# Optimization experiments

Measured on AMD Instinct MI355X. Metric: run time of the kernel, lower is better.

## Reference

```python
import jax, jax.numpy as jnp
import numpy as np

B_, L, D_MODEL = 2, 2048, 1024
EXPAND, D_INNER, D_STATE, DT_RANK, D_CONV = 2, 2048, 16, 64, 4
DT_MIN, DT_MAX = 0.001, 0.1


def setup_inputs() -> dict:
    key = jax.random.key(0)
    ks = jax.random.split(key, 8)
    s = lambda fan: 1.0 / np.sqrt(fan)
    # S4D-real style init for A: A = -exp(A_log), A_log = log(1..n) repeated over d_inner
    A0 = jnp.broadcast_to(jnp.arange(1, D_STATE + 1, dtype=jnp.float32), (D_INNER, D_STATE))
    return {
        "x": jax.random.normal(ks[0], (B_, L, D_MODEL), jnp.float32),
        "W_in": jax.random.normal(ks[1], (D_MODEL, 2 * D_INNER), jnp.float32) * s(D_MODEL),
        "conv_k": jax.random.normal(ks[2], (D_CONV, D_INNER // EXPAND, D_INNER), jnp.float32) * s(D_CONV * D_INNER // EXPAND),
        "conv_b": jnp.zeros((D_INNER,), jnp.float32),
        "W_x": jax.random.normal(ks[3], (D_INNER, DT_RANK + 2 * D_STATE), jnp.float32) * s(D_INNER),
        "W_dt": jax.random.normal(ks[4], (DT_RANK, D_INNER), jnp.float32) * s(DT_RANK),
        "b_dt": jnp.zeros((D_INNER,), jnp.float32),
        "A_log": jnp.log(A0),
        "D": jnp.ones((D_INNER,), jnp.float32),
        "W_out": jax.random.normal(ks[5], (D_INNER, D_MODEL), jnp.float32) * s(D_INNER),
    }


def reference(x, W_in, conv_k, conv_b, W_x, W_dt, b_dt, A_log, D, W_out):
    # in_proj -> split into ssm branch and gating residual branch
    xz = x @ W_in                                   # (b, l, 2*d_inner)
    xs, res = jnp.split(xz, 2, axis=-1)
    # causal grouped conv1d (feature_group_count = expand)
    xc = jax.lax.conv_general_dilated(
        xs, conv_k, window_strides=(1,), padding=[(D_CONV - 1, 0)],
        dimension_numbers=("NWC", "WIO", "NWC"), feature_group_count=EXPAND,
    ) + conv_b
    u = jax.nn.silu(xc)                             # (b, l, d_inner)
    # x_proj -> delta(low-rank), B, C
    dbc = u @ W_x                                   # (b, l, dt_rank + 2n)
    dt_raw = dbc[..., :DT_RANK]
    Bm = dbc[..., DT_RANK:DT_RANK + D_STATE]        # (b, l, n)
    Cm = dbc[..., DT_RANK + D_STATE:]               # (b, l, n)
    delta = jax.nn.softplus(dt_raw @ W_dt + b_dt)   # (b, l, d_inner)
    delta = jnp.clip(delta, DT_MIN, DT_MAX)
    A = -jnp.exp(A_log)                             # (d_inner, n)
    dA = jnp.exp(delta[..., None] * A)              # (b, l, d_inner, n)
    dBu = delta[..., None] * u[..., None] * Bm[:, :, None, :]  # (b, l, d_inner, n)

    def step(h, inp):
        dA_t, dBu_t, C_t = inp                      # (b,d,n),(b,d,n),(b,n)
        h = dA_t * h + dBu_t
        y_t = jnp.einsum('bdn,bn->bd', h, C_t)
        return h, y_t

    h0 = jnp.zeros((x.shape[0], D_INNER, D_STATE), dA.dtype)
    _, y = jax.lax.scan(step, h0, (dA.transpose(1, 0, 2, 3), dBu.transpose(1, 0, 2, 3), Cm.transpose(1, 0, 2)))
    y = y.transpose(1, 0, 2) + u * D                # (b, l, d_inner)
    out = (y * jax.nn.silu(res)) @ W_out            # (b, l, d_model)
    return out
```

## Files before the change

kernel.cpp:

```cpp
#include <hip/hip_runtime.h>
#include <math.h>


typedef unsigned short ushort_t;
typedef unsigned int uint_t;
typedef __bf16 bf16x8 __attribute__((ext_vector_type(8)));
typedef float floatx4 __attribute__((ext_vector_type(4)));

#define LDS_STRIDE 40

#define GLOAD16(gp, lp) \
    __builtin_amdgcn_global_load_lds((const __attribute__((address_space(1))) void*)(gp), \
                                     (__attribute__((address_space(3))) void*)(lp), 16, 0, 0)

__device__ __forceinline__ float silu_f(float x) { return x / (1.0f + __expf(-x)); }

__device__ __forceinline__ unsigned short f2bf(float f) {
    unsigned u = __float_as_uint(f);
    unsigned r = u + 0x7fffu + ((u >> 16) & 1u);
    return (unsigned short)(r >> 16);
}
__device__ __forceinline__ float bf2f(unsigned short h) {
    return __uint_as_float(((unsigned)h) << 16);
}
__device__ __forceinline__ uint_t packhl(float v) {
    const unsigned short h = f2bf(v);
    const unsigned short l = f2bf(v - bf2f(h));
    return (uint_t)h | ((uint_t)l << 16);
}
__device__ __forceinline__ float unpack_sum(uint_t pk) {
    return __uint_as_float(pk << 16) + __uint_as_float(pk & 0xffff0000u);
}
__device__ __forceinline__ void unpack8(uint4 w0, uint4 w1, uint4& H, uint4& L) {
    H.x = (w0.x & 0xffffu) | (w0.y << 16);  L.x = (w0.x >> 16) | (w0.y & 0xffff0000u);
    H.y = (w0.z & 0xffffu) | (w0.w << 16);  L.y = (w0.z >> 16) | (w0.w & 0xffff0000u);
    H.z = (w1.x & 0xffffu) | (w1.y << 16);  L.z = (w1.x >> 16) | (w1.y & 0xffff0000u);
    H.w = (w1.z & 0xffffu) | (w1.w << 16);  L.w = (w1.z >> 16) | (w1.w & 0xffff0000u);
}
__device__ __forceinline__ size_t faddr(int n, int k, int KC) {
    return ((size_t)((n >> 4) * KC + (k >> 5)) * 64 + (n & 15) + (((k >> 3) & 3) << 4)) * 8
           + (k & 7);
}

__global__ __launch_bounds__(256) void prep_all(
    const float* __restrict__ x, const float* __restrict__ W_in,
    const float* __restrict__ conv_k, const float* __restrict__ W_out,
    const float* __restrict__ W_x,
    ushort_t* __restrict__ xh, ushort_t* __restrict__ xl,
    ushort_t* __restrict__ WinF, ushort_t* __restrict__ convkF,
    ushort_t* __restrict__ WoutF, ushort_t* __restrict__ WxF,
    ushort_t* __restrict__ XSP_h)
{
    __shared__ float ts[32][33];
    const int bid = blockIdx.x;
    const int t = threadIdx.x;
    if (bid < 4096) {
        const size_t i4 = ((size_t)bid * 256 + t) * 4;
        float4 v = *(const float4*)&x[i4];
        ushort4 h, l;
        h.x = f2bf(v.x); l.x = f2bf(v.x - bf2f(h.x));
        h.y = f2bf(v.y); l.y = f2bf(v.y - bf2f(h.y));
        h.z = f2bf(v.z); l.z = f2bf(v.z - bf2f(h.z));
        h.w = f2bf(v.w); l.w = f2bf(v.w - bf2f(h.w));
        *(ushort4*)&xh[i4] = h;
        *(ushort4*)&xl[i4] = l;
        return;
    }
    if (bid >= 18432 && bid < 19456) {
        const int idx = (bid - 18432) * 256 + t;
        const int r = idx >> 11, k = idx & 2047;
        float v = (r < 96) ? W_x[(size_t)k * 96 + r] : 0.f;
        WxF[faddr(r, k, 64)] = f2bf(v);
        return;
    }
    if (bid >= 19456) {
        const int idx = (bid - 19456) * 256 + t;
        const int b = idx / 6144, rem = idx % 6144;
        const int lp = rem >> 11, c = rem & 2047;
        XSP_h[((size_t)b * 2051 + lp) * 2048 + c] = 0;
        return;
    }
    const float* src; int R, C, KC; ushort_t* dst; int bx, by;
    if (bid < 8192)       { src = W_in;   R = 1024; C = 4096; KC = 32;  dst = WinF;
                            int l = bid - 4096;  bx = l & 127; by = l >> 7; }
    else if (bid < 16384) { src = conv_k; R = 4096; C = 2048; KC = 128; dst = convkF;
                            int l = bid - 8192;  bx = l & 63;  by = l >> 6; }
    else                  { src = W_out;  R = 2048; C = 1024; KC = 64;  dst = WoutF;
                            int l = bid - 16384; bx = l & 31;  by = l >> 5; }
    const int tx = t & 31, ty = t >> 5;
    const int r0 = by * 32, c0 = bx * 32;
    #pragma unroll
    for (int j = 0; j < 4; ++j)
        ts[ty + j * 8][tx] = src[(size_t)(r0 + ty + j * 8) * C + c0 + tx];
    __syncthreads();
    #pragma unroll
    for (int j = 0; j < 4; ++j) {
        const int n = c0 + ty + j * 8, k = r0 + tx;
        dst[faddr(n, k, KC)] = f2bf(ts[tx][ty + j * 8]);
    }
}

template<int MODE>
__global__ __launch_bounds__(256) void gemm2(
    const uint_t* __restrict__ Apk, const ushort_t* __restrict__ Bf, int Kfull,
    float* __restrict__ Cf, ushort_t* __restrict__ Oh)
{
    __shared__ __align__(16) ushort_t As_h[128 * LDS_STRIDE];
    __shared__ __align__(16) ushort_t As_l[128 * LDS_STRIDE];
    const int t = threadIdx.x;
    int bx, by;
    if (MODE == 2) { bx = blockIdx.x; by = blockIdx.y; }
    else {
        const int lin = blockIdx.x, xcd = lin & 7, s = lin >> 3;
        bx = s >> 2;
        by = xcd * 4 + (s & 3);
    }
    const int m0 = by * 128;
    const int n0 = (MODE == 2) ? 0 : bx * 128;
    const int kbeg = (MODE == 2) ? bx * 512 : 0;
    const int kend = (MODE == 2) ? kbeg + 512 : Kfull;
    const int KC = Kfull >> 5;
    const int lane = t & 63, wave = t >> 6;
    const int wm = (wave >> 1) * 64, wn = (wave & 1) * 64;
    const int m16 = lane & 15, q = lane >> 4;
    const int n16b = (n0 + wn) >> 4;
    const int r_0 = t >> 2, cc_0 = (t & 3) * 8;
    const int r_1 = (t + 256) >> 2, cc_1 = ((t + 256) & 3) * 8;

    uint4 a00 = *(const uint4*)&Apk[(size_t)(m0 + r_0) * Kfull + kbeg + cc_0];
    uint4 a01 = *(const uint4*)&Apk[(size_t)(m0 + r_0) * Kfull + kbeg + cc_0 + 4];
    uint4 a10 = *(const uint4*)&Apk[(size_t)(m0 + r_1) * Kfull + kbeg + cc_1];
    uint4 a11 = *(const uint4*)&Apk[(size_t)(m0 + r_1) * Kfull + kbeg + cc_1 + 4];
    bf16x8 bc[4];
    {
        const int kc = kbeg >> 5;
        #pragma unroll
        for (int j = 0; j < 4; ++j)
            bc[j] = *(const bf16x8*)&Bf[(((size_t)(n16b + j) * KC + kc) * 64 + lane) * 8];
    }

    floatx4 acc[4][4];
    const floatx4 zz = {0.f, 0.f, 0.f, 0.f};
    #pragma unroll
    for (int i = 0; i < 4; ++i)
        #pragma unroll
        for (int j = 0; j < 4; ++j) acc[i][j] = zz;

    for (int k0 = kbeg; k0 < kend; k0 += 32) {
        uint4 H, L;
        unpack8(a00, a01, H, L);
        *(uint4*)&As_h[r_0 * LDS_STRIDE + cc_0] = H;
        *(uint4*)&As_l[r_0 * LDS_STRIDE + cc_0] = L;
        unpack8(a10, a11, H, L);
        *(uint4*)&As_h[r_1 * LDS_STRIDE + cc_1] = H;
        *(uint4*)&As_l[r_1 * LDS_STRIDE + cc_1] = L;
        __syncthreads();
        bf16x8 bn[4];
        if (k0 + 32 < kend) {
            const int kn = k0 + 32, kc = kn >> 5;
            a00 = *(const uint4*)&Apk[(size_t)(m0 + r_0) * Kfull + kn + cc_0];
            a01 = *(const uint4*)&Apk[(size_t)(m0 + r_0) * Kfull + kn + cc_0 + 4];
            a10 = *(const uint4*)&Apk[(size_t)(m0 + r_1) * Kfull + kn + cc_1];
            a11 = *(const uint4*)&Apk[(size_t)(m0 + r_1) * Kfull + kn + cc_1 + 4];
            #pragma unroll
            for (int j = 0; j < 4; ++j)
                bn[j] = *(const bf16x8*)&Bf[(((size_t)(n16b + j) * KC + kc) * 64 + lane) * 8];
        }
        bf16x8 ah[4], al[4];
        #pragma unroll
        for (int i = 0; i < 4; ++i) {
            const int off = (wm + i * 16 + m16) * LDS_STRIDE + q * 8;
            ah[i] = *(const bf16x8*)&As_h[off];
            al[i] = *(const bf16x8*)&As_l[off];
        }
        #pragma unroll
        for (int i = 0; i < 4; ++i)
            #pragma unroll
            for (int j = 0; j < 4; ++j) {
                acc[i][j] = __builtin_amdgcn_mfma_f32_16x16x32_bf16(ah[i], bc[j], acc[i][j], 0, 0, 0);
                acc[i][j] = __builtin_amdgcn_mfma_f32_16x16x32_bf16(al[i], bc[j], acc[i][j], 0, 0, 0);
            }
        #pragma unroll
        for (int j = 0; j < 4; ++j) bc[j] = bn[j];
        __syncthreads();
    }

    float* Cp = (MODE == 2) ? (Cf + (size_t)bx * 393216) : Cf;
    #pragma unroll
    for (int i = 0; i < 4; ++i) {
        const int row_b = m0 + wm + i * 16 + q * 4;
        #pragma unroll
        for (int j = 0; j < 4; ++j) {
            const int col = n0 + wn + j * 16 + m16;
            #pragma unroll
            for (int rr = 0; rr < 4; ++rr) {
                const int row = row_b + rr;
                const float v = acc[i][j][rr];
                if (MODE == 1) {
                    Cp[(size_t)row * 1024 + col] = v;
                } else {
                    if (col < 96) Cp[(size_t)row * 96 + col] = v;
                }
            }
        }
    }
}

__global__ __launch_bounds__(512, 4) void gemm0p(
    const ushort_t* __restrict__ Ahp, const ushort_t* __restrict__ Alp,
    const ushort_t* __restrict__ Bf,
    float* __restrict__ RES, ushort_t* __restrict__ XSP)
{
    __shared__ __align__(16) ushort_t AhS[2][128 * 32];
    __shared__ __align__(16) ushort_t AlS[2][128 * 32];
    __shared__ __align__(16) ushort_t BS[2][8 * 512];
    const int t = threadIdx.x;
    const int lin = blockIdx.x, xcd = lin & 7, s = lin >> 3;
    const int by = (xcd >> 1) * 8 + (s & 7);
    const int bx = (xcd & 1) * 16 + (s >> 3);
    const int m0 = by * 128, n0 = bx * 128;
    const int lane = t & 63, wave = t >> 6;
    const int wm = (wave >> 2) * 64, wn = (wave & 3) * 32;
    const int m16 = lane & 15, q = lane >> 4;
    const int n16base = n0 >> 4;
    const int l16 = lane >> 2;
    const int csA = (lane & 3) ^ ((lane >> 3) & 3);

    auto stageT = [&](int dbuf, int kc) {
        const int r0 = wave * 16;
        const size_t ga = (size_t)(m0 + r0 + l16) * 1024 + kc * 32 + csA * 8;
        GLOAD16(Ahp + ga, &AhS[dbuf][r0 * 32]);
        GLOAD16(Alp + ga, &AlS[dbuf][r0 * 32]);
        const size_t gb = ((size_t)(n16base + wave) * 32 + kc) * 512 + lane * 8;
        GLOAD16(Bf + gb, &BS[dbuf][wave * 512]);
    };

    floatx4 acc[4][2];
    const floatx4 zz = {0.f, 0.f, 0.f, 0.f};
    #pragma unroll
    for (int i = 0; i < 4; ++i)
        #pragma unroll
        for (int j = 0; j < 2; ++j) acc[i][j] = zz;

    stageT(0, 0);
    asm volatile("s_waitcnt vmcnt(0)" ::: "memory");
    __builtin_amdgcn_s_barrier();
    asm volatile("" ::: "memory");

    int cur = 0;
    for (int T = 0; T < 32; ++T) {
        const int nxt = cur ^ 1;
        if (T < 31) {
            stageT(nxt, T + 1);
            asm volatile("s_waitcnt vmcnt(3)" ::: "memory");
        } else {
            asm volatile("s_waitcnt vmcnt(0)" ::: "memory");
        }
        __builtin_amdgcn_s_barrier();
        asm volatile("" ::: "memory");
        bf16x8 ah[4], al[4], bb[2];
        #pragma unroll
        for (int mi = 0; mi < 4; ++mi) {
            const int rr2 = wm + mi * 16 + m16;
            const int ch = q ^ ((m16 >> 1) & 3);
            ah[mi] = *(const bf16x8*)&AhS[cur][rr2 * 32 + ch * 8];
            al[mi] = *(const bf16x8*)&AlS[cur][rr2 * 32 + ch * 8];
        }
        #pragma unroll
        for (int j = 0; j < 2; ++j)
            bb[j] = *(const bf16x8*)&BS[cur][((wn >> 4) + j) * 512 + lane * 8];
        __builtin_amdgcn_s_setprio(1);
        #pragma unroll
        for (int mi = 0; mi < 4; ++mi)
            #pragma unroll
            for (int j = 0; j < 2; ++j) {
                acc[mi][j] = __builtin_amdgcn_mfma_f32_16x16x32_bf16(ah[mi], bb[j], acc[mi][j], 0, 0, 0);
                acc[mi][j] = __builtin_amdgcn_mfma_f32_16x16x32_bf16(al[mi], bb[j], acc[mi][j], 0, 0, 0);
            }
        __builtin_amdgcn_s_setprio(0);
        asm volatile("" ::: "memory");
        __builtin_amdgcn_s_barrier();
        asm volatile("" ::: "memory");
        cur = nxt;
    }

    #pragma unroll
    for (int i = 0; i < 4; ++i) {
        const int row_b = m0 + wm + i * 16 + q * 4;
        #pragma unroll
        for (int j = 0; j < 2; ++j) {
            const int col = n0 + wn + j * 16 + m16;
            #pragma unroll
            for (int rr = 0; rr < 4; ++rr) {
                const int row = row_b + rr;
                const float v = acc[i][j][rr];
                if (n0 < 2048) {
                    const int b = row >> 11, l = row & 2047;
                    XSP[((size_t)b * 2051 + l + 3) * 2048 + col] = f2bf(v);
                } else {
                    RES[(size_t)row * 2048 + (col - 2048)] = v;
                }
            }
        }
    }
}

__global__ __launch_bounds__(512, 4) void conv2(
    const ushort_t* __restrict__ Xh, const ushort_t* __restrict__ Bf,
    const float* __restrict__ bias, uint_t* __restrict__ Upk)
{
    __shared__ __align__(16) ushort_t Asw[2][2][128 * 32];
    __shared__ __align__(16) ushort_t Bsw[2][2][8 * 512];
    const int t = threadIdx.x;
    const int lin = blockIdx.x, xcd = lin & 7, s = lin >> 3;
    const int by  = (xcd >> 1) * 8 + (s & 7);
    const int bxp = (xcd & 1) * 8 + (s >> 3);
    const int m0 = by * 128, n0 = bxp * 128;
    const int g1024 = (n0 >= 1024) ? 1024 : 0;
    const int lane = t & 63, wave = t >> 6;
    const int wm = (wave >> 2) * 64, wn = (wave & 3) * 32;
    const int m16 = lane & 15, q = lane >> 4;
    const int n16base = n0 >> 4;
    const int Xrow0 = (m0 >> 11) * 2051 + (m0 & 2047);
    const int l16 = lane >> 2;
    const int csA = (lane & 3) ^ ((lane >> 3) & 3);

    auto stageT = [&](int dbuf, int kcL, int Tn) {
        const int wtap = Tn >> 4;
        const int i0 = ((Tn << 6) & 1023) + kcL * 32;
        const int kc = Tn * 2 + kcL;
        {
            const int r0 = wave * 16;
            const size_t gidx = (size_t)(Xrow0 + r0 + l16 + wtap) * 2048
                              + g1024 + i0 + csA * 8;
            GLOAD16(Xh + gidx, &Asw[dbuf][kcL][r0 * 32]);
        }
        {
            const size_t gidx = ((size_t)(n16base + wave) * 128 + kc) * 512 + lane * 8;
            GLOAD16(Bf + gidx, &Bsw[dbuf][kcL][wave * 512]);
        }
    };

    floatx4 acc[4][2];
    const floatx4 zz = {0.f, 0.f, 0.f, 0.f};
    #pragma unroll
    for (int i = 0; i < 4; ++i)
        #pragma unroll
        for (int j = 0; j < 2; ++j) acc[i][j] = zz;

    bf16x8 a0[4], b0[2], a1[4], b1[2];

    auto readA = [&](int dbuf, int kcL, bf16x8 (&ah)[4]) {
        #pragma unroll
        for (int mi = 0; mi < 4; ++mi) {
            const int rr2 = wm + mi * 16 + m16;
            const int ch = q ^ ((m16 >> 1) & 3);
            ah[mi] = *(const bf16x8*)&Asw[dbuf][kcL][rr2 * 32 + ch * 8];
        }
    };
    auto readB = [&](int dbuf, int kcL, bf16x8 (&bb)[2]) {
        #pragma unroll
        for (int j = 0; j < 2; ++j)
            bb[j] = *(const bf16x8*)&Bsw[dbuf][kcL][((wn >> 4) + j) * 512 + lane * 8];
    };
    auto mfma8 = [&](bf16x8 (&ah)[4], bf16x8 (&bb)[2]) {
        __builtin_amdgcn_s_setprio(1);
        #pragma unroll
        for (int mi = 0; mi < 4; ++mi)
            #pragma unroll
            for (int j = 0; j < 2; ++j)
                acc[mi][j] = __builtin_amdgcn_mfma_f32_16x16x32_bf16(ah[mi], bb[j], acc[mi][j], 0, 0, 0);
        __builtin_amdgcn_s_setprio(0);
    };

    stageT(0, 0, 0);
    stageT(0, 1, 0);
    asm volatile("s_waitcnt vmcnt(2)" ::: "memory");
    __builtin_amdgcn_s_barrier();
    asm volatile("" ::: "memory");
    readA(0, 0, a0); readB(0, 0, b0);

    int cur = 0;
    for (int T = 0; T < 64; ++T) {
        const int nxt = cur ^ 1;
        if (T < 63) {
            stageT(nxt, 0, T + 1);
            asm volatile("s_waitcnt vmcnt(2)" ::: "memory");
        } else {
            asm volatile("s_waitcnt vmcnt(0)" ::: "memory");
        }
        __builtin_amdgcn_s_barrier();
        asm volatile("" ::: "memory");
        readA(cur, 1, a1); readB(cur, 1, b1);
        mfma8(a0, b0);
        if (T < 63) stageT(nxt, 1, T + 1);
        mfma8(a1, b1);
        asm volatile("" ::: "memory");
        if (T < 63) {
            asm volatile("s_waitcnt vmcnt(2)" ::: "memory");
            __builtin_amdgcn_s_barrier();
            asm volatile("" ::: "memory");
            readA(nxt, 0, a0); readB(nxt, 0, b0);
        }
        cur = nxt;
    }

    #pragma unroll
    for (int i = 0; i < 4; ++i) {
        const int row_b = m0 + wm + i * 16 + q * 4;
        #pragma unroll
        for (int j = 0; j < 2; ++j) {
            const int col = n0 + wn + j * 16 + m16;
            const float bz = bias[col];
            #pragma unroll
            for (int rr = 0; rr < 4; ++rr) {
                const int row = row_b + rr;
                const float v = silu_f(acc[i][j][rr] + bz);
                Upk[(size_t)row * 2048 + col] = packhl(v);
            }
        }
    }
}

__global__ __launch_bounds__(256) void dbc_reduce(
    const float* __restrict__ DBCP, float* __restrict__ DBC)
{
    const int i = blockIdx.x * 256 + threadIdx.x;
    DBC[i] = (DBCP[i] + DBCP[393216 + i]) + (DBCP[786432 + i] + DBCP[1179648 + i]);
}

__global__ __launch_bounds__(256) void delta_kernel(
    const float* __restrict__ DBC, const float* __restrict__ W_dt,
    const float* __restrict__ b_dt, float* __restrict__ DELTA)
{
    const int n  = blockIdx.x * 256 + threadIdx.x;
    const int p0 = blockIdx.y * 16;
    const int t  = threadIdx.x;
    __shared__ float dt_s[16][64];
    #pragma unroll
    for (int j = 0; j < 4; ++j) {
        const int lin = j * 256 + t;
        const int r = lin >> 6, k = lin & 63;
        dt_s[r][k] = DBC[(size_t)(p0 + r) * 96 + k];
    }
    __syncthreads();
    float acc[16];
    const float bz = b_dt[n];
    #pragma unroll
    for (int r = 0; r < 16; ++r) acc[r] = bz;
    for (int k = 0; k < 64; ++k) {
        const float wv = W_dt[(size_t)k * 2048 + n];
        #pragma unroll
        for (int r = 0; r < 16; ++r) acc[r] += dt_s[r][k] * wv;
    }
    #pragma unroll
    for (int r = 0; r < 16; ++r) {
        float a = acc[r];
        float sp = (a > 20.f) ? a : log1pf(expf(a));
        sp = fminf(fmaxf(sp, 0.001f), 0.1f);
        DELTA[(size_t)(p0 + r) * 2048 + n] = sp;
    }
}

__global__ __launch_bounds__(256) void scan_p1(
    const float* __restrict__ DELTA, const uint_t* __restrict__ Upk,
    const float* __restrict__ DBC, const float* __restrict__ A_log,
    float* __restrict__ HEND, float* __restrict__ SD)
{
    const int t = threadIdx.x;
    const int d = blockIdx.x * 256 + t;
    const int c = blockIdx.y;
    const int b = blockIdx.z;
    const int p0 = b * 2048 + c * 32;
    __shared__ float Bs[32][16];
    for (int lin = t; lin < 512; lin += 256) {
        const int s = lin >> 4, n = lin & 15;
        Bs[s][n] = DBC[(size_t)(p0 + s) * 96 + 64 + n];
    }
    __syncthreads();
    float Af[16];
    *(float4*)&Af[0]  = *(const float4*)&A_log[(size_t)d * 16 + 0];
    *(float4*)&Af[4]  = *(const float4*)&A_log[(size_t)d * 16 + 4];
    *(float4*)&Af[8]  = *(const float4*)&A_log[(size_t)d * 16 + 8];
    *(float4*)&Af[12] = *(const float4*)&A_log[(size_t)d * 16 + 12];
    #pragma unroll
    for (int n = 0; n < 16; ++n) Af[n] = -__expf(Af[n]);

    float h[16] = {};
    float sd = 0.f;
    for (int s = 0; s < 32; ++s) {
        const size_t ix = (size_t)(p0 + s) * 2048 + d;
        const float dv = DELTA[ix];
        const float uv = unpack_sum(Upk[ix]);
        const float du = dv * uv;
        sd += dv;
        #pragma unroll
        for (int n = 0; n < 16; ++n)
            h[n] = __expf(dv * Af[n]) * h[n] + du * Bs[s][n];
    }
    const size_t hb = (((size_t)c * 2 + b) * 2048 + d) * 16;
    *(float4*)&HEND[hb + 0]  = *(float4*)&h[0];
    *(float4*)&HEND[hb + 4]  = *(float4*)&h[4];
    *(float4*)&HEND[hb + 8]  = *(float4*)&h[8];
    *(float4*)&HEND[hb + 12] = *(float4*)&h[12];
    SD[((size_t)c * 2 + b) * 2048 + d] = sd;
}

__global__ __launch_bounds__(256) void scan_p2(
    const float* __restrict__ HEND, const float* __restrict__ SD,
    const float* __restrict__ A_log, float* __restrict__ HINIT)
{
    const int g = blockIdx.x * 256 + threadIdx.x;
    const int n = g & 15, d = (g >> 4) & 2047, b = (g >> 15) & 1;
    const float Af = -__expf(A_log[(size_t)d * 16 + n]);
    float h = 0.f;
    #pragma unroll 8
    for (int c = 0; c < 64; ++c) {
        const size_t cb = (size_t)c * 2 + b;
        const size_t idx = (cb * 2048 + d) * 16 + n;
        HINIT[idx] = h;
        h = __expf(Af * SD[cb * 2048 + d]) * h + HEND[idx];
    }
}

__global__ __launch_bounds__(256) void scan_p3(
    const float* __restrict__ DELTA, const uint_t* __restrict__ Upk,
    const float* __restrict__ DBC, const float* __restrict__ RES,
    const float* __restrict__ A_log, const float* __restrict__ Dp,
    const float* __restrict__ HINIT, uint_t* __restrict__ Gpk)
{
    const int t = threadIdx.x;
    const int d = blockIdx.x * 256 + t;
    const int c = blockIdx.y;
    const int b = blockIdx.z;
    const int p0 = b * 2048 + c * 32;
    __shared__ float Bs[32][16];
    __shared__ float Cs[32][16];
    for (int lin = t; lin < 512; lin += 256) {
        const int s = lin >> 4, n = lin & 15;
        Bs[s][n] = DBC[(size_t)(p0 + s) * 96 + 64 + n];
        Cs[s][n] = DBC[(size_t)(p0 + s) * 96 + 80 + n];
    }
    __syncthreads();
    float Af[16];
    *(float4*)&Af[0]  = *(const float4*)&A_log[(size_t)d * 16 + 0];
    *(float4*)&Af[4]  = *(const float4*)&A_log[(size_t)d * 16 + 4];
    *(float4*)&Af[8]  = *(const float4*)&A_log[(size_t)d * 16 + 8];
    *(float4*)&Af[12] = *(const float4*)&A_log[(size_t)d * 16 + 12];
    #pragma unroll
    for (int n = 0; n < 16; ++n) Af[n] = -__expf(Af[n]);

    const size_t hb = (((size_t)c * 2 + b) * 2048 + d) * 16;
    float h[16];
    *(float4*)&h[0]  = *(const float4*)&HINIT[hb + 0];
    *(float4*)&h[4]  = *(const float4*)&HINIT[hb + 4];
    *(float4*)&h[8]  = *(const float4*)&HINIT[hb + 8];
    *(float4*)&h[12] = *(const float4*)&HINIT[hb + 12];
    const float Dd = Dp[d];

    for (int s = 0; s < 32; ++s) {
        const int p = p0 + s;
        const size_t ix = (size_t)p * 2048 + d;
        const float dv = DELTA[ix];
        const float uv = unpack_sum(Upk[ix]);
        const float du = dv * uv;
        float y = 0.f;
        #pragma unroll
        for (int n = 0; n < 16; ++n) {
            h[n] = __expf(dv * Af[n]) * h[n] + du * Bs[s][n];
            y += h[n] * Cs[s][n];
        }
        const float resv = RES[ix];
        const float gv = (y + uv * Dd) * silu_f(resv);
        Gpk[ix] = packhl(gv);
    }
}

extern "C" void kernel_launch(void* const* d_in, const int* in_sizes, int n_in,
                              void* d_out, int out_size, void* d_ws, size_t ws_size,
                              hipStream_t stream) {
    const float* x      = (const float*)d_in[0];
    const float* W_in   = (const float*)d_in[1];
    const float* conv_k = (const float*)d_in[2];
    const float* conv_b = (const float*)d_in[3];
    const float* W_x    = (const float*)d_in[4];
    const float* W_dt   = (const float*)d_in[5];
    const float* b_dt   = (const float*)d_in[6];
    const float* A_log  = (const float*)d_in[7];
    const float* Dv     = (const float*)d_in[8];
    const float* W_out  = (const float*)d_in[9];
    float* out = (float*)d_out;

    char* base = (char*)d_ws;
    float*    RES      = (float*)(base);
    uint_t*   Upk      = (uint_t*)(base + 33554432);
    float*    DELTA    = (float*)(base + 67108864);
    ushort_t* XSP_h    = (ushort_t*)(base + 100663296);
    float*    HEND     = (float*)(base + 100663296);
    ushort_t* xh       = (ushort_t*)(base + 117465088);
    ushort_t* xl       = (ushort_t*)(base + 125853696);
    ushort_t* convkF   = (ushort_t*)(base + 134242304);
    uint_t*   Gpk      = (uint_t*)(base + 117465088);
    ushort_t* WinF     = (ushort_t*)(base + 151019520);
    ushort_t* WoutF    = (ushort_t*)(base + 159408128);
    ushort_t* WxF      = (ushort_t*)(base + 163602432);
    float*    DBCP     = (float*)(base + 164126720);
    float*    DBC      = (float*)(base + 170418176);
    float*    SD       = (float*)(base + 171991040);
    float*    HINIT    = (float*)(base + 173039616);

    prep_all<<<19504, 256, 0, stream>>>(x, W_in, conv_k, W_out, W_x,
                                        xh, xl, WinF, convkF, WoutF, WxF, XSP_h);
    gemm0p<<<1024, 512, 0, stream>>>(xh, xl, WinF, RES, XSP_h);
    conv2<<<512, 512, 0, stream>>>(XSP_h, convkF, conv_b, Upk);
    gemm2<2><<<dim3(4, 32), 256, 0, stream>>>(Upk, WxF, 2048, DBCP, nullptr);
    dbc_reduce<<<1536, 256, 0, stream>>>(DBCP, DBC);
    delta_kernel<<<dim3(8, 256), 256, 0, stream>>>(DBC, W_dt, b_dt, DELTA);
    scan_p1<<<dim3(8, 64, 2), 256, 0, stream>>>(DELTA, Upk, DBC, A_log, HEND, SD);
    scan_p2<<<256, 256, 0, stream>>>(HEND, SD, A_log, HINIT);
    scan_p3<<<dim3(8, 64, 2), 256, 0, stream>>>(DELTA, Upk, DBC, RES, A_log, Dv,
                                                HINIT, Gpk);
    gemm2<1><<<256, 256, 0, stream>>>(Gpk, WoutF, 2048, out, nullptr);
}
```

Before: 473.8 us.

## Replace output projection GEMM with split-K MFMA kernel and separate hi/lo planes

The output projection now uses a new gemm1p kernel modeled on the input-projection GEMM. It uses 128x128 tiles, a split-K of 2 over 512 blocks and async global-to-LDS loads, writes partial sums that out_reduce adds together, and replaces the previous gemm2<1> launch. scan_p3 now writes separate bf16 hi and lo arrays instead of packed words so they can be streamed straight into LDS. The gemm0p wave layout is also changed to 32x64 per wave (2x4 fragments instead of 4x2), which changes LDS read reuse. The split-K adds a 32 MB partial buffer write plus an extra reduction launch.

```diff
diff --git a/kernel.cpp b/kernel.cpp
--- a/kernel.cpp
+++ b/kernel.cpp
@@ -220,7 +220,7 @@
     const int bx = (xcd & 1) * 16 + (s >> 3);
     const int m0 = by * 128, n0 = bx * 128;
     const int lane = t & 63, wave = t >> 6;
-    const int wm = (wave >> 2) * 64, wn = (wave & 3) * 32;
+    const int wm = (wave & 3) * 32, wn = (wave >> 2) * 64;
     const int m16 = lane & 15, q = lane >> 4;
     const int n16base = n0 >> 4;
     const int l16 = lane >> 2;
@@ -235,12 +235,12 @@
         GLOAD16(Bf + gb, &BS[dbuf][wave * 512]);
     };
 
-    floatx4 acc[4][2];
+    floatx4 acc[2][4];
     const floatx4 zz = {0.f, 0.f, 0.f, 0.f};
     #pragma unroll
-    for (int i = 0; i < 4; ++i)
-        #pragma unroll
-        for (int j = 0; j < 2; ++j) acc[i][j] = zz;
+    for (int i = 0; i < 2; ++i)
+        #pragma unroll
+        for (int j = 0; j < 4; ++j) acc[i][j] = zz;
 
     stageT(0, 0);
     asm volatile("s_waitcnt vmcnt(0)" ::: "memory");
@@ -258,22 +258,22 @@
         }
         __builtin_amdgcn_s_barrier();
         asm volatile("" ::: "memory");
-        bf16x8 ah[4], al[4], bb[2];
-        #pragma unroll
-        for (int mi = 0; mi < 4; ++mi) {
+        bf16x8 ah[2], al[2], bb[4];
+        #pragma unroll
+        for (int mi = 0; mi < 2; ++mi) {
             const int rr2 = wm + mi * 16 + m16;
             const int ch = q ^ ((m16 >> 1) & 3);
             ah[mi] = *(const bf16x8*)&AhS[cur][rr2 * 32 + ch * 8];
             al[mi] = *(const bf16x8*)&AlS[cur][rr2 * 32 + ch * 8];
         }
         #pragma unroll
-        for (int j = 0; j < 2; ++j)
+        for (int j = 0; j < 4; ++j)
             bb[j] = *(const bf16x8*)&BS[cur][((wn >> 4) + j) * 512 + lane * 8];
         __builtin_amdgcn_s_setprio(1);
         #pragma unroll
-        for (int mi = 0; mi < 4; ++mi)
-            #pragma unroll
-            for (int j = 0; j < 2; ++j) {
+        for (int mi = 0; mi < 2; ++mi)
+            #pragma unroll
+            for (int j = 0; j < 4; ++j) {
                 acc[mi][j] = __builtin_amdgcn_mfma_f32_16x16x32_bf16(ah[mi], bb[j], acc[mi][j], 0, 0, 0);
                 acc[mi][j] = __builtin_amdgcn_mfma_f32_16x16x32_bf16(al[mi], bb[j], acc[mi][j], 0, 0, 0);
             }
@@ -285,10 +285,10 @@
     }
 
     #pragma unroll
-    for (int i = 0; i < 4; ++i) {
+    for (int i = 0; i < 2; ++i) {
         const int row_b = m0 + wm + i * 16 + q * 4;
         #pragma unroll
-        for (int j = 0; j < 2; ++j) {
+        for (int j = 0; j < 4; ++j) {
             const int col = n0 + wn + j * 16 + m16;
             #pragma unroll
             for (int rr = 0; rr < 4; ++rr) {
@@ -303,6 +303,113 @@
             }
         }
     }
+}
+
+__global__ __launch_bounds__(512, 4) void gemm1p(
+    const ushort_t* __restrict__ Ghp, const ushort_t* __restrict__ Glp,
+    const ushort_t* __restrict__ Bf, float* __restrict__ PO)
+{
+    __shared__ __align__(16) ushort_t AhS[2][128 * 32];
+    __shared__ __align__(16) ushort_t AlS[2][128 * 32];
+    __shared__ __align__(16) ushort_t BS[2][8 * 512];
+    const int t = threadIdx.x;
+    const int lin = blockIdx.x, xcd = lin & 7, s = lin >> 3;
+    const int ks = s >> 5;
+    const int r = s & 31;
+    const int by = (xcd >> 1) * 8 + (r & 7);
+    const int bx = (xcd & 1) * 4 + (r >> 3);
+    const int m0 = by * 128, n0 = bx * 128;
+    const int lane = t & 63, wave = t >> 6;
+    const int wm = (wave & 3) * 32, wn = (wave >> 2) * 64;
+    const int m16 = lane & 15, q = lane >> 4;
+    const int n16base = n0 >> 4;
+    const int l16 = lane >> 2;
+    const int csA = (lane & 3) ^ ((lane >> 3) & 3);
+    const int kc0 = ks * 32;
+
+    auto stageT = [&](int dbuf, int kc) {
+        const int r0 = wave * 16;
+        const size_t ga = (size_t)(m0 + r0 + l16) * 2048 + kc * 32 + csA * 8;
+        GLOAD16(Ghp + ga, &AhS[dbuf][r0 * 32]);
+        GLOAD16(Glp + ga, &AlS[dbuf][r0 * 32]);
+        const size_t gb = ((size_t)(n16base + wave) * 64 + kc) * 512 + lane * 8;
+        GLOAD16(Bf + gb, &BS[dbuf][wave * 512]);
+    };
+
+    floatx4 acc[2][4];
+    const floatx4 zz = {0.f, 0.f, 0.f, 0.f};
+    #pragma unroll
+    for (int i = 0; i < 2; ++i)
+        #pragma unroll
+        for (int j = 0; j < 4; ++j) acc[i][j] = zz;
+
+    stageT(0, kc0);
+    asm volatile("s_waitcnt vmcnt(0)" ::: "memory");
+    __builtin_amdgcn_s_barrier();
+    asm volatile("" ::: "memory");
+
+    int cur = 0;
+    for (int T = 0; T < 32; ++T) {
+        const int nxt = cur ^ 1;
+        if (T < 31) {
+            stageT(nxt, kc0 + T + 1);
+            asm volatile("s_waitcnt vmcnt(3)" ::: "memory");
+        } else {
+            asm volatile("s_waitcnt vmcnt(0)" ::: "memory");
+        }
+        __builtin_amdgcn_s_barrier();
+        asm volatile("" ::: "memory");
+        bf16x8 ah[2], al[2], bb[4];
+        #pragma unroll
+        for (int mi = 0; mi < 2; ++mi) {
+            const int rr2 = wm + mi * 16 + m16;
+            const int ch = q ^ ((m16 >> 1) & 3);
+            ah[mi] = *(const bf16x8*)&AhS[cur][rr2 * 32 + ch * 8];
+            al[mi] = *(const bf16x8*)&AlS[cur][rr2 * 32 + ch * 8];
+        }
+        #pragma unroll
+        for (int j = 0; j < 4; ++j)
+            bb[j] = *(const bf16x8*)&BS[cur][((wn >> 4) + j) * 512 + lane * 8];
+        __builtin_amdgcn_s_setprio(1);
+        #pragma unroll
+        for (int mi = 0; mi < 2; ++mi)
+            #pragma unroll
+            for (int j = 0; j < 4; ++j) {
+                acc[mi][j] = __builtin_amdgcn_mfma_f32_16x16x32_bf16(ah[mi], bb[j], acc[mi][j], 0, 0, 0);
+                acc[mi][j] = __builtin_amdgcn_mfma_f32_16x16x32_bf16(al[mi], bb[j], acc[mi][j], 0, 0, 0);
+            }
+        __builtin_amdgcn_s_setprio(0);
+        asm volatile("" ::: "memory");
+        __builtin_amdgcn_s_barrier();
+        asm volatile("" ::: "memory");
+        cur = nxt;
+    }
+
+    float* Cp = PO + (size_t)ks * 4194304;
+    #pragma unroll
+    for (int i = 0; i < 2; ++i) {
+        const int row_b = m0 + wm + i * 16 + q * 4;
+        #pragma unroll
+        for (int j = 0; j < 4; ++j) {
+            const int col = n0 + wn + j * 16 + m16;
+            #pragma unroll
+            for (int rr = 0; rr < 4; ++rr) {
+                const int row = row_b + rr;
+                Cp[(size_t)row * 1024 + col] = acc[i][j][rr];
+            }
+        }
+    }
+}
+
+__global__ __launch_bounds__(256) void out_reduce(
+    const float* __restrict__ PO, float* __restrict__ out)
+{
+    const int i = (blockIdx.x * 256 + threadIdx.x) * 4;
+    float4 a = *(const float4*)&PO[i];
+    float4 b = *(const float4*)&PO[4194304 + i];
+    float4 rv;
+    rv.x = a.x + b.x; rv.y = a.y + b.y; rv.z = a.z + b.z; rv.w = a.w + b.w;
+    *(float4*)&out[i] = rv;
 }
 
 __global__ __launch_bounds__(512, 4) void conv2(
@@ -527,7 +634,8 @@
     const float* __restrict__ DELTA, const uint_t* __restrict__ Upk,
     const float* __restrict__ DBC, const float* __restrict__ RES,
     const float* __restrict__ A_log, const float* __restrict__ Dp,
-    const float* __restrict__ HINIT, uint_t* __restrict__ Gpk)
+    const float* __restrict__ HINIT,
+    ushort_t* __restrict__ Gh, ushort_t* __restrict__ Gl)
 {
     const int t = threadIdx.x;
     const int d = blockIdx.x * 256 + t;
@@ -572,7 +680,9 @@
         }
         const float resv = RES[ix];
         const float gv = (y + uv * Dd) * silu_f(resv);
-        Gpk[ix] = packhl(gv);
+        const unsigned short hh = f2bf(gv);
+        Gh[ix] = hh;
+        Gl[ix] = f2bf(gv - bf2f(hh));
     }
 }
 
@@ -595,12 +705,14 @@
     float*    RES      = (float*)(base);
     uint_t*   Upk      = (uint_t*)(base + 33554432);
     float*    DELTA    = (float*)(base + 67108864);
+    float*    PO       = (float*)(base + 67108864);
     ushort_t* XSP_h    = (ushort_t*)(base + 100663296);
     float*    HEND     = (float*)(base + 100663296);
     ushort_t* xh       = (ushort_t*)(base + 117465088);
     ushort_t* xl       = (ushort_t*)(base + 125853696);
     ushort_t* convkF   = (ushort_t*)(base + 134242304);
-    uint_t*   Gpk      = (uint_t*)(base + 117465088);
+    ushort_t* Gh       = (ushort_t*)(base + 117465088);
+    ushort_t* Gl       = (ushort_t*)(base + 134242304);
     ushort_t* WinF     = (ushort_t*)(base + 151019520);
     ushort_t* WoutF    = (ushort_t*)(base + 159408128);
     ushort_t* WxF      = (ushort_t*)(base + 163602432);
@@ -619,6 +731,7 @@
     scan_p1<<<dim3(8, 64, 2), 256, 0, stream>>>(DELTA, Upk, DBC, A_log, HEND, SD);
     scan_p2<<<256, 256, 0, stream>>>(HEND, SD, A_log, HINIT);
     scan_p3<<<dim3(8, 64, 2), 256, 0, stream>>>(DELTA, Upk, DBC, RES, A_log, Dv,
-                                                HINIT, Gpk);
-    gemm2<1><<<256, 256, 0, stream>>>(Gpk, WoutF, 2048, out, nullptr);
-}
+                                                HINIT, Gh, Gl);
+    gemm1p<<<512, 512, 0, stream>>>(Gh, Gl, WoutF, PO);
+    out_reduce<<<4096, 256, 0, stream>>>(PO, out);
+}
```

New measurement: 453.9 us. -4.2%, faster.
